# Kernel tuning notes

Hardware: AMD Instinct MI355X
Metric: run time of the kernel (lower is better)

The kernel has to match this reference:

```python
import jax, jax.numpy as jnp
import numpy as np

B, LQ, LD, H, DIM, PF = 16, 64, 2048, 1024, 128, 4
MAXK = LD // PF + 1  # static upper bound on num clusters (valid_len <= LD)


def setup_inputs() -> dict:
    key = jax.random.key(0)
    k1, k2, k3, k4 = jax.random.split(key, 4)
    return {
        "q_hidden": jax.random.normal(k1, (B, LQ, H), jnp.float32),
        "d_hidden": jax.random.normal(k2, (B, LD, H), jnp.float32),
        "W": jax.random.normal(k3, (H, DIM), jnp.float32) * (1.0 / np.sqrt(H)),  # xavier-ish
        "b": jnp.zeros((DIM,), jnp.float32),
        "q_mask": jnp.ones((B, LQ), jnp.int32),
        "d_mask": jnp.ones((B, LD), jnp.int32),
        "labels": jax.random.randint(k4, (B, LD), 0, MAXK, dtype=jnp.int32),
        "pooling_factor": PF,
    }


def _encode(hidden, W, b, mask):
    # proj -> L2 normalize -> zero out padded tokens
    r = hidden @ W + b
    r = r / jnp.clip(jnp.linalg.norm(r, axis=-1, keepdims=True), 1e-12)
    return r * mask[..., None].astype(r.dtype)


def _pool(d_repr, d_mask, labels, pf):
    # segment-mean per batch sample, cluster labels supplied externally
    Bn, L, D = d_repr.shape
    max_k = L // pf + 1  # static
    valid = jnp.clip(d_mask.sum(-1), 2, None)          # [B]
    k = valid // pf + 1                                 # per-sample num clusters
    lab = jnp.where(d_mask > 0, labels % k[:, None], max_k)  # invalid tokens -> dummy seg
    seg = lambda vals, idx: jax.ops.segment_sum(vals, idx, num_segments=max_k + 1)
    sums = jax.vmap(seg)(d_repr, lab)[:, :max_k]                          # [B,K,D]
    counts = jax.vmap(seg)(jnp.where(d_mask > 0, 1.0, 0.0), lab)[:, :max_k]
    means = sums / jnp.clip(counts, 1.0)[..., None]
    means = means / jnp.clip(jnp.linalg.norm(means, axis=-1, keepdims=True), 1e-12)
    pad_mask = jnp.arange(max_k)[None, :] < k[:, None]                    # [B,K]
    return means * pad_mask[..., None], pad_mask


def reference(q_hidden, d_hidden, W, b, q_mask, d_mask, labels, pooling_factor):
    q = _encode(q_hidden, W, b, q_mask)            # [B,LQ,DIM]
    d = _encode(d_hidden, W, b, d_mask)            # [B,LD,DIM]
    d_pool, pmask = _pool(d, d_mask, labels, pooling_factor)  # [B,K,DIM]
    sim = jnp.einsum('bqd,bkd->bqk', q, d_pool)
    sim = jnp.where(pmask[:, None, :], sim, -1e4)
    score = (sim.max(-1) * q_mask.astype(sim.dtype)).sum(-1)  # maxsum per pair
    return score
```

## Files before the change

### kernel.cpp

```cpp
#include <hip/hip_runtime.h>
#include <hip/hip_bf16.h>

#define BB    16
#define LQ    64
#define LD    2048
#define HH    1024
#define DIM   128
#define MAXK  513
#define SCH   9
#define DGRID 1024
#define QGRID 32

typedef __attribute__((ext_vector_type(8))) short short8;
typedef __attribute__((ext_vector_type(4))) float f32x4;

__device__ __forceinline__ float b2f(ushort u) {
    union { float f; unsigned int u32; } c; c.u32 = ((unsigned int)u) << 16; return c.f;
}
__device__ __forceinline__ ushort f2b_rn(float f) {
    unsigned int x = __float_as_uint(f);
    return (ushort)((x + 0x7fffu + ((x >> 16) & 1u)) >> 16);
}

__device__ __forceinline__ void gld16(void* lds, const void* g) {
    __builtin_amdgcn_global_load_lds(
        (const __attribute__((address_space(1))) unsigned int*)g,
        (__attribute__((address_space(3))) unsigned int*)lds,
        16, 0, 0);
}

__global__ __launch_bounds__(256) void prep_kb_kernel(
    const float* __restrict__ W,
    const int*   __restrict__ d_mask,
    const int*   __restrict__ pf,
    ushort*      __restrict__ Wt,
    int*         __restrict__ kvals)
{
    __shared__ int red[4];
    int bid = blockIdx.x, t = threadIdx.x;
    if (bid < 512) {
        int idx = bid * 256 + t;
        int h = idx >> 7;
        int n = idx & 127;
        Wt[n * HH + h] = f2b_rn(W[idx]);
    } else {
        int b = bid - 512;
        int lane = t & 63, wave = t >> 6;
        int s = 0;
        for (int i = t; i < LD; i += 256) s += (d_mask[b * LD + i] > 0) ? 1 : 0;
        #pragma unroll
        for (int m = 1; m < 64; m <<= 1) s += __shfl_xor(s, m);
        if (lane == 0) red[wave] = s;
        __syncthreads();
        if (t == 0) {
            int v = red[0] + red[1] + red[2] + red[3];
            if (v < 2) v = 2;
            int pfv = pf[0];
            if (pfv < 1 || pfv > LD) pfv = 4;
            kvals[b] = v / pfv + 1;
        }
    }
}

__global__ __launch_bounds__(256, 4) void encode_kernel(
    const float*  __restrict__ Xd,
    const float*  __restrict__ Xq,
    const ushort* __restrict__ Wt,
    const float*  __restrict__ bias,
    const int*    __restrict__ mask_d,
    const int*    __restrict__ mask_q,
    const int*    __restrict__ labels,
    const int*    __restrict__ kvals,
    float*        __restrict__ sums,
    float*        __restrict__ q_repr)
{
    __shared__ __align__(16) uint4 buf[2][768];
    __shared__ float ssh[32][2];

    const int bid = blockIdx.x;
    const bool isq = bid >= DGRID;
    const float* X = isq ? Xq : Xd;
    const long row0 = isq ? (long)(bid - DGRID) * 32 : (long)bid * 32;

    const int t = threadIdx.x;
    const int w = t >> 6, lane = t & 63;
    const int m16 = lane & 15, quad = lane >> 4;
    const int rh = w & 1, ch = w >> 1;

    const float*  gA  = X + (row0 + w * 8 + (lane >> 3)) * HH
                          + (((lane & 7) ^ ((lane >> 3) & 7)) * 4);
    const ushort* gB0 = Wt + (long)(w * 32 + (lane >> 2)) * HH
                           + (((lane & 3) ^ ((lane >> 4) & 3)) * 8);
    const ushort* gB1 = gB0 + 16 * HH;

    f32x4 acc[4];
    #pragma unroll
    for (int j = 0; j < 4; ++j) acc[j] = (f32x4){0.f, 0.f, 0.f, 0.f};

    gld16(&buf[0][w * 64], gA);
    gld16(&buf[0][256 + w * 128], gB0);
    gld16(&buf[0][256 + w * 128 + 64], gB1);

    const int sw = m16 & 7;
    const int bsw = m16 >> 2;
    const int au = (rh * 16 + m16) * 8;

    for (int c = 0; c < 32; ++c) {
        __syncthreads();
        const int cur = c & 1;

        if (c < 31) {
            const int nxt = cur ^ 1;
            const int ko = (c + 1) * 32;
            gld16(&buf[nxt][w * 64], gA + ko);
            gld16(&buf[nxt][256 + w * 128], gB0 + ko);
            gld16(&buf[nxt][256 + w * 128 + 64], gB1 + ko);
        }

        float4 va0 = *(const float4*)&buf[cur][au + ((2 * quad) ^ sw)];
        float4 va1 = *(const float4*)&buf[cur][au + ((2 * quad + 1) ^ sw)];
        float av[8];
        *(float4*)(av) = va0; *(float4*)(av + 4) = va1;
        short8 ah, al;
        #pragma unroll
        for (int j = 0; j < 8; ++j) {
            unsigned int ux = __float_as_uint(av[j]);
            ah[j] = (short)(ux >> 16);
            float hif = __uint_as_float(ux & 0xffff0000u);
            al[j] = (short)(__float_as_uint(av[j] - hif) >> 16);
        }

        #pragma unroll
        for (int cti = 0; cti < 4; ++cti) {
            const int ct = ch * 4 + cti;
            short8 bf = *(const short8*)&buf[cur][256 + (ct * 16 + m16) * 4 + (quad ^ bsw)];
            acc[cti] = __builtin_amdgcn_mfma_f32_16x16x32_bf16(ah, bf, acc[cti], 0, 0, 0);
            acc[cti] = __builtin_amdgcn_mfma_f32_16x16x32_bf16(al, bf, acc[cti], 0, 0, 0);
        }
    }

    float bia[4];
    #pragma unroll
    for (int cti = 0; cti < 4; ++cti) bia[cti] = bias[(ch * 4 + cti) * 16 + m16];

    float vv[4][4];
    float ssp[4] = {0.f, 0.f, 0.f, 0.f};
    #pragma unroll
    for (int cti = 0; cti < 4; ++cti)
        #pragma unroll
        for (int r = 0; r < 4; ++r) {
            vv[cti][r] = acc[cti][r] + bia[cti];
            ssp[r] += vv[cti][r] * vv[cti][r];
        }
    #pragma unroll
    for (int r = 0; r < 4; ++r) {
        ssp[r] += __shfl_xor(ssp[r], 1);
        ssp[r] += __shfl_xor(ssp[r], 2);
        ssp[r] += __shfl_xor(ssp[r], 4);
        ssp[r] += __shfl_xor(ssp[r], 8);
    }
    if (m16 == 0) {
        #pragma unroll
        for (int r = 0; r < 4; ++r) ssh[rh * 16 + quad * 4 + r][ch] = ssp[r];
    }
    __syncthreads();

    #pragma unroll
    for (int r = 0; r < 4; ++r) {
        int rowl = rh * 16 + quad * 4 + r;
        long rowg = row0 + rowl;
        float ss = ssh[rowl][0] + ssh[rowl][1];
        float scale = 1.0f / fmaxf(sqrtf(ss), 1e-12f);
        if (isq) {
            scale *= (float)mask_q[rowg];
            #pragma unroll
            for (int cti = 0; cti < 4; ++cti)
                q_repr[rowg * DIM + (ch * 4 + cti) * 16 + m16] = vv[cti][r] * scale;
        } else if (mask_d[rowg] > 0) {
            int b = (int)(rowg >> 11);
            int seg = labels[rowg] % kvals[b];
            float* sp = sums + ((long)b * MAXK + seg) * DIM + m16;
            #pragma unroll
            for (int cti = 0; cti < 4; ++cti)
                atomicAdd(sp + (ch * 4 + cti) * 16, vv[cti][r] * scale);
        }
    }
}

__global__ __launch_bounds__(256) void simmax_kernel(
    const float* __restrict__ q_repr,
    const float* __restrict__ sums,
    const int*   __restrict__ kvals,
    float*       __restrict__ pmax)
{
    __shared__ __align__(16) ushort Qh[64 * 136];
    __shared__ __align__(16) ushort Ql[64 * 136];
    __shared__ __align__(16) ushort Ch[64 * 136];
    __shared__ float cn[64];

    int b = blockIdx.x / SCH, chunk = blockIdx.x % SCH;
    int t = threadIdx.x, w = t >> 6, lane = t & 63;
    int m16 = lane & 15, quad = lane >> 4;

    #pragma unroll
    for (int i = 0; i < 8; ++i) {
        int flat = i * 256 + t;
        int row = flat >> 5, c4 = flat & 31;
        float4 v = *(const float4*)(q_repr + ((long)b * LQ + row) * DIM + c4 * 4);
        float x[4]; *(float4*)x = v;
        ushort4 h, l;
        ushort* hp = (ushort*)&h; ushort* lp = (ushort*)&l;
        #pragma unroll
        for (int j = 0; j < 4; ++j) {
            unsigned int ux = __float_as_uint(x[j]);
            hp[j] = (ushort)(ux >> 16);
            lp[j] = f2b_rn(x[j] - __uint_as_float(ux & 0xffff0000u));
        }
        *(ushort4*)&Qh[row * 136 + c4 * 4] = h;
        *(ushort4*)&Ql[row * 136 + c4 * 4] = l;
    }
    #pragma unroll
    for (int i = 0; i < 8; ++i) {
        int flat = i * 256 + t;
        int row = flat >> 5, c4 = flat & 31;
        int kk = chunk * 64 + row;
        float4 v = (kk < MAXK)
            ? *(const float4*)(sums + ((long)b * MAXK + kk) * DIM + c4 * 4)
            : make_float4(0.f, 0.f, 0.f, 0.f);
        ushort4 h; ushort* hp = (ushort*)&h;
        hp[0] = f2b_rn(v.x); hp[1] = f2b_rn(v.y);
        hp[2] = f2b_rn(v.z); hp[3] = f2b_rn(v.w);
        *(ushort4*)&Ch[row * 136 + c4 * 4] = h;
    }
    __syncthreads();

    {
        int c = w * 16 + m16;
        float ssv = 0.f;
        #pragma unroll
        for (int j = 0; j < 16; ++j) {
            unsigned int u = *(const unsigned int*)&Ch[c * 136 + quad * 32 + j * 2];
            float x0 = b2f((ushort)u), x1 = b2f((ushort)(u >> 16));
            ssv += x0 * x0 + x1 * x1;
        }
        ssv += __shfl_xor(ssv, 16);
        ssv += __shfl_xor(ssv, 32);
        if (quad == 0) cn[c] = (ssv > 1e-24f) ? rsqrtf(ssv) : 0.f;
    }
    __syncthreads();

    f32x4 acc[4];
    #pragma unroll
    for (int j = 0; j < 4; ++j) acc[j] = (f32x4){0.f, 0.f, 0.f, 0.f};

    #pragma unroll
    for (int kc = 0; kc < 4; ++kc) {
        short8 qh = *(const short8*)&Qh[(w * 16 + m16) * 136 + kc * 32 + quad * 8];
        short8 ql = *(const short8*)&Ql[(w * 16 + m16) * 136 + kc * 32 + quad * 8];
        #pragma unroll
        for (int ct = 0; ct < 4; ++ct) {
            short8 cf = *(const short8*)&Ch[(ct * 16 + m16) * 136 + kc * 32 + quad * 8];
            acc[ct] = __builtin_amdgcn_mfma_f32_16x16x32_bf16(qh, cf, acc[ct], 0, 0, 0);
            acc[ct] = __builtin_amdgcn_mfma_f32_16x16x32_bf16(ql, cf, acc[ct], 0, 0, 0);
        }
    }

    int kb = kvals[b];
    #pragma unroll
    for (int r = 0; r < 4; ++r) {
        float mx = -1e4f;
        #pragma unroll
        for (int ct = 0; ct < 4; ++ct) {
            int cl = chunk * 64 + ct * 16 + m16;
            float sim = acc[ct][r] * cn[ct * 16 + m16];
            mx = fmaxf(mx, (cl < kb) ? sim : -1e4f);
        }
        mx = fmaxf(mx, __shfl_xor(mx, 1));
        mx = fmaxf(mx, __shfl_xor(mx, 2));
        mx = fmaxf(mx, __shfl_xor(mx, 4));
        mx = fmaxf(mx, __shfl_xor(mx, 8));
        if (m16 == 0)
            pmax[((long)b * SCH + chunk) * 64 + w * 16 + quad * 4 + r] = mx;
    }
}

__global__ __launch_bounds__(64) void final_kernel(
    const float* __restrict__ pmax,
    const int*   __restrict__ q_mask,
    float*       __restrict__ out)
{
    int b = blockIdx.x, r = threadIdx.x;
    float m = -3e38f;
    #pragma unroll
    for (int c = 0; c < SCH; ++c)
        m = fmaxf(m, pmax[((long)b * SCH + c) * 64 + r]);
    m *= (float)q_mask[b * LQ + r];
    #pragma unroll
    for (int sh = 1; sh < 64; sh <<= 1) m += __shfl_xor(m, sh);
    if (r == 0) out[b] = m;
}

extern "C" void kernel_launch(void* const* d_in, const int* in_sizes, int n_in,
                              void* d_out, int out_size, void* d_ws, size_t ws_size,
                              hipStream_t stream) {
    const float* q_hidden = (const float*)d_in[0];
    const float* d_hidden = (const float*)d_in[1];
    const float* W        = (const float*)d_in[2];
    const float* bias     = (const float*)d_in[3];
    const int*   q_mask   = (const int*)d_in[4];
    const int*   d_mask   = (const int*)d_in[5];
    const int*   labels   = (const int*)d_in[6];
    const int*   pf       = (const int*)d_in[7];

    float* ws     = (float*)d_ws;
    float* q_repr = ws;
    float* sums   = q_repr + (long)BB * LQ * DIM;
    float* pmaxb  = sums + (long)BB * MAXK * DIM;
    int*   kvals  = (int*)(pmaxb + BB * SCH * 64);
    ushort* Wt    = (ushort*)(kvals + 16);

    hipMemsetAsync(sums, 0, (size_t)BB * MAXK * DIM * sizeof(float), stream);

    prep_kb_kernel<<<512 + BB, 256, 0, stream>>>(W, d_mask, pf, Wt, kvals);
    encode_kernel<<<DGRID + QGRID, 256, 0, stream>>>(d_hidden, q_hidden, Wt, bias,
                                                     d_mask, q_mask, labels, kvals,
                                                     sums, q_repr);
    simmax_kernel<<<BB * SCH, 256, 0, stream>>>(q_repr, sums, kvals, pmaxb);
    final_kernel<<<BB, 64, 0, stream>>>(pmaxb, q_mask, (float*)d_out);
}
```

Before: 256.9 us.

## Give each wave private LDS staging and drop per-iteration block barriers in encode GEMM

The encode GEMM main loop now has each wave load only the A rows and W columns it consumes into its own LDS region. Block-wide __syncthreads are replaced by per-wave vmcnt waits, and prefetch runs two chunks ahead. This removes the cross-wave barrier stalls every K-step and deepens the load pipeline, at the cost of redundant global loads (A and B tiles each fetched by two waves) and more LDS, so occupancy is lowered to 3 blocks per SM.

Result: slower. 279.7 us (+8.9%).

```diff
diff --git a/kernel.cpp b/kernel.cpp
--- a/kernel.cpp
+++ b/kernel.cpp
@@ -13,6 +13,9 @@
 
 typedef __attribute__((ext_vector_type(8))) short short8;
 typedef __attribute__((ext_vector_type(4))) float f32x4;
+
+#define WC_VM6 0x0F76
+#define WC_VM0 0x0F70
 
 __device__ __forceinline__ float b2f(ushort u) {
     union { float f; unsigned int u32; } c; c.u32 = ((unsigned int)u) << 16; return c.f;
@@ -62,7 +65,7 @@
     }
 }
 
-__global__ __launch_bounds__(256, 4) void encode_kernel(
+__global__ __launch_bounds__(256, 3) void encode_kernel(
     const float*  __restrict__ Xd,
     const float*  __restrict__ Xq,
     const ushort* __restrict__ Wt,
@@ -74,7 +77,7 @@
     float*        __restrict__ sums,
     float*        __restrict__ q_repr)
 {
-    __shared__ __align__(16) uint4 buf[2][768];
+    __shared__ __align__(16) uint4 buf[4 * 768];
     __shared__ float ssh[32][2];
 
     const int bid = blockIdx.x;
@@ -85,40 +88,50 @@
     const int t = threadIdx.x;
     const int w = t >> 6, lane = t & 63;
     const int m16 = lane & 15, quad = lane >> 4;
-    const int rh = w & 1, ch = w >> 1;
-
-    const float*  gA  = X + (row0 + w * 8 + (lane >> 3)) * HH
+    const int rg = w & 1, cg = w >> 1;
+    const int wbase = w * 768;
+
+    const float*  gA0 = X + (row0 + rg * 16 + (lane >> 3)) * HH
                           + (((lane & 7) ^ ((lane >> 3) & 7)) * 4);
-    const ushort* gB0 = Wt + (long)(w * 32 + (lane >> 2)) * HH
-                           + (((lane & 3) ^ ((lane >> 4) & 3)) * 8);
+    const float*  gA1 = gA0 + 8 * HH;
+    const ushort* gB0 = Wt + (long)(cg * 64 + (lane >> 2)) * HH
+                           + (((lane & 3) ^ ((lane >> 3) & 3)) * 8);
     const ushort* gB1 = gB0 + 16 * HH;
+    const ushort* gB2 = gB0 + 32 * HH;
+    const ushort* gB3 = gB0 + 48 * HH;
+
+    auto stage = [&](int slot, int chunk) {
+        const int ko = chunk * 32;
+        uint4* s = &buf[wbase + slot * 384];
+        gld16(s +   0, gA0 + ko);
+        gld16(s +  64, gA1 + ko);
+        gld16(s + 128, gB0 + ko);
+        gld16(s + 192, gB1 + ko);
+        gld16(s + 256, gB2 + ko);
+        gld16(s + 320, gB3 + ko);
+    };
 
     f32x4 acc[4];
     #pragma unroll
     for (int j = 0; j < 4; ++j) acc[j] = (f32x4){0.f, 0.f, 0.f, 0.f};
 
-    gld16(&buf[0][w * 64], gA);
-    gld16(&buf[0][256 + w * 128], gB0);
-    gld16(&buf[0][256 + w * 128 + 64], gB1);
+    stage(0, 0);
+    stage(1, 1);
 
     const int sw = m16 & 7;
-    const int bsw = m16 >> 2;
-    const int au = (rh * 16 + m16) * 8;
-
+    const int bk = (m16 >> 1) & 3;
+
+    #pragma unroll 4
     for (int c = 0; c < 32; ++c) {
-        __syncthreads();
-        const int cur = c & 1;
-
-        if (c < 31) {
-            const int nxt = cur ^ 1;
-            const int ko = (c + 1) * 32;
-            gld16(&buf[nxt][w * 64], gA + ko);
-            gld16(&buf[nxt][256 + w * 128], gB0 + ko);
-            gld16(&buf[nxt][256 + w * 128 + 64], gB1 + ko);
-        }
-
-        float4 va0 = *(const float4*)&buf[cur][au + ((2 * quad) ^ sw)];
-        float4 va1 = *(const float4*)&buf[cur][au + ((2 * quad + 1) ^ sw)];
+        __builtin_amdgcn_sched_barrier(0);
+        if (c < 31) __builtin_amdgcn_s_waitcnt(WC_VM6);
+        else        __builtin_amdgcn_s_waitcnt(WC_VM0);
+        __builtin_amdgcn_sched_barrier(0);
+
+        const uint4* sl = &buf[wbase + (c & 1) * 384];
+
+        float4 va0 = *(const float4*)&sl[m16 * 8 + ((2 * quad)     ^ sw)];
+        float4 va1 = *(const float4*)&sl[m16 * 8 + ((2 * quad + 1) ^ sw)];
         float av[8];
         *(float4*)(av) = va0; *(float4*)(av + 4) = va1;
         short8 ah, al;
@@ -131,26 +144,28 @@
         }
 
         #pragma unroll
-        for (int cti = 0; cti < 4; ++cti) {
-            const int ct = ch * 4 + cti;
-            short8 bf = *(const short8*)&buf[cur][256 + (ct * 16 + m16) * 4 + (quad ^ bsw)];
-            acc[cti] = __builtin_amdgcn_mfma_f32_16x16x32_bf16(ah, bf, acc[cti], 0, 0, 0);
-            acc[cti] = __builtin_amdgcn_mfma_f32_16x16x32_bf16(al, bf, acc[cti], 0, 0, 0);
-        }
+        for (int ct = 0; ct < 4; ++ct) {
+            short8 bf = *(const short8*)&sl[128 + (ct * 16 + m16) * 4 + (quad ^ bk)];
+            acc[ct] = __builtin_amdgcn_mfma_f32_16x16x32_bf16(ah, bf, acc[ct], 0, 0, 0);
+            acc[ct] = __builtin_amdgcn_mfma_f32_16x16x32_bf16(al, bf, acc[ct], 0, 0, 0);
+        }
+
+        __builtin_amdgcn_sched_barrier(0);
+        if (c < 30) stage(c & 1, c + 2);
     }
 
     float bia[4];
     #pragma unroll
-    for (int cti = 0; cti < 4; ++cti) bia[cti] = bias[(ch * 4 + cti) * 16 + m16];
+    for (int ct = 0; ct < 4; ++ct) bia[ct] = bias[cg * 64 + ct * 16 + m16];
 
     float vv[4][4];
     float ssp[4] = {0.f, 0.f, 0.f, 0.f};
     #pragma unroll
-    for (int cti = 0; cti < 4; ++cti)
+    for (int ct = 0; ct < 4; ++ct)
         #pragma unroll
         for (int r = 0; r < 4; ++r) {
-            vv[cti][r] = acc[cti][r] + bia[cti];
-            ssp[r] += vv[cti][r] * vv[cti][r];
+            vv[ct][r] = acc[ct][r] + bia[ct];
+            ssp[r] += vv[ct][r] * vv[ct][r];
         }
     #pragma unroll
     for (int r = 0; r < 4; ++r) {
@@ -161,28 +176,28 @@
     }
     if (m16 == 0) {
         #pragma unroll
-        for (int r = 0; r < 4; ++r) ssh[rh * 16 + quad * 4 + r][ch] = ssp[r];
+        for (int r = 0; r < 4; ++r) ssh[rg * 16 + quad * 4 + r][cg] = ssp[r];
     }
     __syncthreads();
 
     #pragma unroll
     for (int r = 0; r < 4; ++r) {
-        int rowl = rh * 16 + quad * 4 + r;
+        int rowl = rg * 16 + quad * 4 + r;
         long rowg = row0 + rowl;
         float ss = ssh[rowl][0] + ssh[rowl][1];
         float scale = 1.0f / fmaxf(sqrtf(ss), 1e-12f);
         if (isq) {
             scale *= (float)mask_q[rowg];
             #pragma unroll
-            for (int cti = 0; cti < 4; ++cti)
-                q_repr[rowg * DIM + (ch * 4 + cti) * 16 + m16] = vv[cti][r] * scale;
+            for (int ct = 0; ct < 4; ++ct)
+                q_repr[rowg * DIM + cg * 64 + ct * 16 + m16] = vv[ct][r] * scale;
         } else if (mask_d[rowg] > 0) {
             int b = (int)(rowg >> 11);
             int seg = labels[rowg] % kvals[b];
-            float* sp = sums + ((long)b * MAXK + seg) * DIM + m16;
+            float* sp = sums + ((long)b * MAXK + seg) * DIM + cg * 64 + m16;
             #pragma unroll
-            for (int cti = 0; cti < 4; ++cti)
-                atomicAdd(sp + (ch * 4 + cti) * 16, vv[cti][r] * scale);
+            for (int ct = 0; ct < 4; ++ct)
+                atomicAdd(sp + ct * 16, vv[ct][r] * scale);
         }
     }
 }
```
